# Performance work log

Measured on AMD Instinct MI355X. Metric: run time of the kernel, lower is better.

## Reference

```python
import jax, jax.numpy as jnp
import numpy as np

N_IN = 512
N_OUT = 256
T = 2048
B = 32


def setup_inputs() -> dict:
    key = jax.random.key(0)
    ks = jax.random.split(key, 9)
    s_in = 1.0 / np.sqrt(N_IN)
    inp = {
        "xt": jax.random.normal(ks[0], (T, B, N_IN), dtype=jnp.float32),
        "ct_forward": jax.random.normal(ks[1], (1, B, N_OUT), dtype=jnp.float32),
        # weights stored torch-style as [out, in]
        "Wx": jax.random.uniform(ks[2], (N_OUT, N_IN), jnp.float32, -s_in, s_in),
        "Wf": jax.random.uniform(ks[3], (N_OUT, N_IN), jnp.float32, -s_in, s_in),
        "bf": jax.random.uniform(ks[4], (N_OUT,), jnp.float32, -s_in, s_in),
        "Wr": jax.random.uniform(ks[5], (N_OUT, N_IN), jnp.float32, -s_in, s_in),
        "br": jax.random.uniform(ks[6], (N_OUT,), jnp.float32, -s_in, s_in),
        "Wc": jax.random.uniform(ks[7], (N_OUT, N_IN), jnp.float32, -s_in, s_in),
        "bc": jax.random.uniform(ks[8], (N_OUT,), jnp.float32, -s_in, s_in),
    }
    return inp


def reference(xt, ct_forward, Wx, Wf, bf, Wr, br, Wc, bc):
    # Batched projections over all timesteps (the GEMM part of SRU).
    x_proj = jnp.einsum("tbi,oi->tbo", xt, Wx)              # [T,B,n_out]
    f = jax.nn.sigmoid(jnp.einsum("tbi,oi->tbo", xt, Wf) + bf)
    r = jax.nn.sigmoid(jnp.einsum("tbi,oi->tbo", xt, Wr) + br)
    cx = jnp.einsum("tbi,oi->tbo", xt, Wc) + bc

    def step(c, inp):
        x_t, ft, rt, cxt = inp
        c = ft * c + (1.0 - ft) * x_t
        h = rt * jnp.tanh(c) + (1.0 - rt) * cxt
        return c, h

    c_final, ht = jax.lax.scan(step, ct_forward[0], (x_proj, f, r, cx))
    # dropout=0.0 -> identity; forward returns (ht, ct)
    return ht, c_final
```

## Files before the change

### kernel.cpp

```cpp
#include <hip/hip_runtime.h>
#include <stdint.h>

#define T_STEPS 2048
#define BATCH   32
#define NIN     512
#define NOUT    256
#define MROWS   (T_STEPS*BATCH)
#define BO      (BATCH*NOUT)
#define NCHUNK  32
#define CHLEN   (T_STEPS/NCHUNK)

typedef _Float16 f16x8 __attribute__((ext_vector_type(8)));
typedef _Float16 f16x4 __attribute__((ext_vector_type(4)));
typedef float    fx4   __attribute__((ext_vector_type(4)));

#define LDSP(p) ((__attribute__((address_space(3))) void*)(p))
#define GLBP(p) ((const __attribute__((address_space(1))) void*)(p))

#define BAR()       asm volatile("s_barrier" ::: "memory")
#define WAITLGKM0() do { asm volatile("s_waitcnt lgkmcnt(0)" ::: "memory"); __builtin_amdgcn_sched_barrier(0); } while(0)
#define WAITVM(n)   do { asm volatile("s_waitcnt vmcnt(" #n ")" ::: "memory"); __builtin_amdgcn_sched_barrier(0); } while(0)

__global__ __launch_bounds__(256) void convert_x(
    const float* __restrict__ xt, _Float16* __restrict__ xh)
{
    long i = ((long)blockIdx.x * 256 + threadIdx.x) * 8;
    float4 v0 = *(const float4*)(xt + i);
    float4 v1 = *(const float4*)(xt + i + 4);
    f16x8 h;
    h[0] = (_Float16)v0.x; h[1] = (_Float16)v0.y;
    h[2] = (_Float16)v0.z; h[3] = (_Float16)v0.w;
    h[4] = (_Float16)v1.x; h[5] = (_Float16)v1.y;
    h[6] = (_Float16)v1.z; h[7] = (_Float16)v1.w;
    *(f16x8*)(xh + i) = h;
}

__global__ __launch_bounds__(256) void convert_w(
    const float* __restrict__ Wx, const float* __restrict__ Wf,
    const float* __restrict__ Wr, const float* __restrict__ Wc,
    _Float16* __restrict__ Wcat)
{
    int idx = blockIdx.x * 256 + threadIdx.x;
    int n  = idx >> 7;
    int k4 = (idx & 127) * 4;
    int g = n >> 8, o = n & 255;
    const float* W = (g == 0) ? Wx : (g == 1) ? Wf : (g == 2) ? Wr : Wc;
    float4 v = *(const float4*)(W + o * NIN + k4);
    f16x4 h;
    h[0] = (_Float16)v.x; h[1] = (_Float16)v.y;
    h[2] = (_Float16)v.z; h[3] = (_Float16)v.w;
    *(f16x4*)(Wcat + n * NIN + k4) = h;
}

#define BM 256
#define BN 256
#define BK 64
#define NKT (NIN / BK)

__global__ __launch_bounds__(512) void gemm_proj(
    const _Float16* __restrict__ xh,
    const _Float16* __restrict__ Wcat,
    const float* __restrict__ bfv, const float* __restrict__ brv, const float* __restrict__ bcv,
    _Float16* __restrict__ xp_h, _Float16* __restrict__ f_h,
    _Float16* __restrict__ r_h,  _Float16* __restrict__ cx_h)
{
    __shared__ char lds[131072];

    const int tid  = threadIdx.x;
    const int lane = tid & 63;
    const int w    = tid >> 6;
    const int wrq  = w >> 2;
    const int wcq  = w & 3;
    const int lr = lane & 15, lk = lane >> 4;

    int wg = (blockIdx.x & 7) * 128 + (blockIdx.x >> 3);
    const int  rowblk = wg >> 2;
    const int  cg     = wg & 3;
    const long m0 = (long)rowblk * BM;
    const int  n0 = cg * BN;

    const int rl8  = lane >> 3;
    const int scol = (((lane & 7) ^ rl8) << 4);
    const char* baseA = (const char*)xh   + (m0 + w * 8 + rl8) * 1024 + scol;
    const char* baseB = (const char*)Wcat + ((long)(n0 + w * 8 + rl8)) * 1024 + scol;

#define STAGE_A(t, h) do {                                                   \
        char* _d = lds + ((t) & 1) * 32768 + (h) * 16384 + w * 1024;         \
        const char* _s = baseA + (long)(h) * 131072 + (t) * 128;             \
        __builtin_amdgcn_global_load_lds(GLBP(_s),         LDSP(_d),        16, 0, 0); \
        __builtin_amdgcn_global_load_lds(GLBP(_s + 65536), LDSP(_d + 8192), 16, 0, 0); \
    } while (0)
#define STAGE_B(t, h) do {                                                   \
        char* _d = lds + 65536 + ((t) & 1) * 32768 + (h) * 16384 + w * 1024; \
        const char* _s = baseB + (long)(h) * 131072 + (t) * 128;             \
        __builtin_amdgcn_global_load_lds(GLBP(_s),         LDSP(_d),        16, 0, 0); \
        __builtin_amdgcn_global_load_lds(GLBP(_s + 65536), LDSP(_d + 8192), 16, 0, 0); \
    } while (0)

    fx4 acc[2][2][4][2];
    #pragma unroll
    for (int a = 0; a < 2; ++a)
        #pragma unroll
        for (int b = 0; b < 2; ++b)
            #pragma unroll
            for (int c = 0; c < 4; ++c)
                #pragma unroll
                for (int d = 0; d < 2; ++d)
                    acc[a][b][c][d] = (fx4){0.f, 0.f, 0.f, 0.f};

    f16x8 Ar[4][2];
    f16x8 B0r[2][2];
    f16x8 B1r[2][2];

#define READ_A(c2, h) do {                                                   \
        _Pragma("unroll")                                                    \
        for (int mf = 0; mf < 4; ++mf) {                                     \
            int rl = wrq * 64 + mf * 16 + lr;                                \
            int rb = (c2) * 32768 + (h) * 16384 + rl * 128;                  \
            _Pragma("unroll")                                                \
            for (int kk = 0; kk < 2; ++kk)                                   \
                Ar[mf][kk] = *(const f16x8*)(lds + rb +                      \
                    ((kk * 64 + lk * 16) ^ ((rl & 7) << 4)));                \
        }                                                                    \
    } while (0)
#define READ_B(c2, h, dst) do {                                              \
        _Pragma("unroll")                                                    \
        for (int nf = 0; nf < 2; ++nf) {                                     \
            int rl = wcq * 32 + nf * 16 + lr;                                \
            int rb = 65536 + (c2) * 32768 + (h) * 16384 + rl * 128;          \
            _Pragma("unroll")                                                \
            for (int kk = 0; kk < 2; ++kk)                                   \
                dst[nf][kk] = *(const f16x8*)(lds + rb +                     \
                    ((kk * 64 + lk * 16) ^ ((rl & 7) << 4)));                \
        }                                                                    \
    } while (0)
#define MMACC(Qr, Qc, Br) do {                                               \
        __builtin_amdgcn_s_setprio(1);                                       \
        _Pragma("unroll")                                                    \
        for (int kk = 0; kk < 2; ++kk)                                       \
            _Pragma("unroll")                                                \
            for (int mf = 0; mf < 4; ++mf)                                   \
                _Pragma("unroll")                                            \
                for (int nf = 0; nf < 2; ++nf)                               \
                    acc[Qr][Qc][mf][nf] = __builtin_amdgcn_mfma_f32_16x16x32_f16( \
                        Ar[mf][kk], Br[nf][kk], acc[Qr][Qc][mf][nf], 0, 0, 0);    \
        __builtin_amdgcn_s_setprio(0);                                       \
    } while (0)

    STAGE_A(0, 0); STAGE_B(0, 0); STAGE_B(0, 1); STAGE_A(0, 1);
    STAGE_A(1, 0); STAGE_B(1, 0);
    WAITVM(4);
    BAR();

    for (int t = 0; t < NKT; ++t) {
        const int c2 = t & 1;
        READ_A(c2, 0);
        READ_B(c2, 0, B0r);
        if (t + 1 < NKT) STAGE_B(t + 1, 1);
        BAR();
        WAITLGKM0();
        MMACC(0, 0, B0r);
        BAR();
        READ_B(c2, 1, B1r);
        if (t + 1 < NKT) STAGE_A(t + 1, 1);
        BAR();
        WAITLGKM0();
        MMACC(0, 1, B1r);
        BAR();
        READ_A(c2, 1);
        if (t + 2 < NKT) STAGE_A(t + 2, 0);
        BAR();
        WAITLGKM0();
        MMACC(1, 0, B0r);
        BAR();
        if (t + 2 < NKT) STAGE_B(t + 2, 0);
        BAR();
        MMACC(1, 1, B1r);
        if (t < NKT - 2)       WAITVM(4);
        else if (t == NKT - 2) WAITVM(0);
        BAR();
    }

    const int g = cg;
    _Float16* outp = (g == 0) ? xp_h : (g == 1) ? f_h : (g == 2) ? r_h : cx_h;
    const float* bias = (g == 1) ? bfv : (g == 2) ? brv : (g == 3) ? bcv : nullptr;
    #pragma unroll
    for (int Qr = 0; Qr < 2; ++Qr) {
        #pragma unroll
        for (int Qc = 0; Qc < 2; ++Qc) {
            #pragma unroll
            for (int mf = 0; mf < 4; ++mf) {
                #pragma unroll
                for (int nf = 0; nf < 2; ++nf) {
                    int o = Qc * 128 + wcq * 32 + nf * 16 + lr;
                    float bv = (g == 0) ? 0.f : bias[o];
                    #pragma unroll
                    for (int j = 0; j < 4; ++j) {
                        long row = m0 + Qr * 128 + wrq * 64 + mf * 16 + lk * 4 + j;
                        float v = acc[Qr][Qc][mf][nf][j] + bv;
                        _Float16 hv;
                        if (g == 1 || g == 2) {
                            float e = __expf(-v);
                            hv = (_Float16)(__builtin_amdgcn_rcpf(1.0f + e));
                        } else {
                            hv = (_Float16)v;
                        }
                        outp[row * NOUT + o] = hv;
                    }
                }
            }
        }
    }
}

__global__ __launch_bounds__(256) void chunk_scan_a(
    const _Float16* __restrict__ f_h, const _Float16* __restrict__ xp_h,
    float* __restrict__ chunkA, float* __restrict__ chunkB)
{
    int tid = blockIdx.x * 256 + threadIdx.x;
    int chunk = tid >> 13;
    int bo = tid & (BO - 1);
    long base = (long)chunk * CHLEN * BO + bo;
    float a = 1.f, cc = 0.f;
    #pragma unroll 4
    for (int s = 0; s < CHLEN; ++s) {
        long i = base + (long)s * BO;
        float fv = (float)f_h[i];
        float xv = (float)xp_h[i];
        cc = fv * cc + (1.f - fv) * xv;
        a *= fv;
    }
    chunkA[tid] = a;
    chunkB[tid] = cc;
}

__global__ __launch_bounds__(256) void chunk_prop(
    const float* __restrict__ ct0,
    const float* __restrict__ chunkA, const float* __restrict__ chunkB,
    float* __restrict__ cin, float* __restrict__ c_final)
{
    int bo = blockIdx.x * 256 + threadIdx.x;
    float c = ct0[bo];
    #pragma unroll
    for (int ch = 0; ch < NCHUNK; ++ch) {
        cin[ch * BO + bo] = c;
        c = chunkA[ch * BO + bo] * c + chunkB[ch * BO + bo];
    }
    c_final[bo] = c;
}

__global__ __launch_bounds__(256) void chunk_scan_h(
    const _Float16* __restrict__ xp_h, const _Float16* __restrict__ f_h,
    const _Float16* __restrict__ r_h,  const _Float16* __restrict__ cx_h,
    const float* __restrict__ cin, float* __restrict__ ht)
{
    int tid = blockIdx.x * 256 + threadIdx.x;
    int chunk = tid >> 13;
    int bo = tid & (BO - 1);
    long base = (long)chunk * CHLEN * BO + bo;
    float c = cin[tid];
    #pragma unroll 4
    for (int s = 0; s < CHLEN; ++s) {
        long i = base + (long)s * BO;
        float fv = (float)f_h[i];
        float xv = (float)xp_h[i];
        float rv = (float)r_h[i];
        float cxv = (float)cx_h[i];
        c = fv * c + (1.f - fv) * xv;
        float e = __expf(2.f * c);
        float th = (e - 1.f) * __builtin_amdgcn_rcpf(e + 1.f);
        ht[i] = rv * th + (1.f - rv) * cxv;
    }
}

extern "C" void kernel_launch(void* const* d_in, const int* in_sizes, int n_in,
                              void* d_out, int out_size, void* d_ws, size_t ws_size,
                              hipStream_t stream) {
    const float* xt  = (const float*)d_in[0];
    const float* ct0 = (const float*)d_in[1];
    const float* Wx  = (const float*)d_in[2];
    const float* Wf  = (const float*)d_in[3];
    const float* bf_ = (const float*)d_in[4];
    const float* Wr  = (const float*)d_in[5];
    const float* br_ = (const float*)d_in[6];
    const float* Wc  = (const float*)d_in[7];
    const float* bc_ = (const float*)d_in[8];

    float* ht      = (float*)d_out;
    float* c_final = ht + (size_t)MROWS * NOUT;

    char* ws = (char*)d_ws;
    _Float16* Wcat = (_Float16*)ws;
    _Float16* xh   = (_Float16*)(ws + (1 << 20));
    _Float16* xp_h = xh + (size_t)MROWS * NIN;
    _Float16* f_h  = xp_h + (size_t)MROWS * NOUT;
    _Float16* r_h  = f_h  + (size_t)MROWS * NOUT;
    _Float16* cx_h = r_h  + (size_t)MROWS * NOUT;
    float* chunkA  = (float*)(cx_h + (size_t)MROWS * NOUT);
    float* chunkB  = chunkA + NCHUNK * BO;
    float* cin     = chunkB + NCHUNK * BO;

    convert_w<<<512, 256, 0, stream>>>(Wx, Wf, Wr, Wc, Wcat);
    convert_x<<<(MROWS * NIN / 8) / 256, 256, 0, stream>>>(xt, xh);
    gemm_proj<<<(MROWS / BM) * 4, 512, 0, stream>>>(
        xh, Wcat, bf_, br_, bc_, xp_h, f_h, r_h, cx_h);
    chunk_scan_a<<<(NCHUNK * BO) / 256, 256, 0, stream>>>(f_h, xp_h, chunkA, chunkB);
    chunk_prop<<<BO / 256, 256, 0, stream>>>(ct0, chunkA, chunkB, cin, c_final);
    chunk_scan_h<<<(NCHUNK * BO) / 256, 256, 0, stream>>>(xp_h, f_h, r_h, cx_h, cin, ht);
}
```

Baseline: 194.5 us.

## Make GEMM persistent over four row tiles and vectorize epilogue stores

The projection GEMM now launches 256 workgroups, each walking four consecutive 256-row tiles with one continuous software pipeline across tile boundaries, writing results and zeroing accumulators every eight k-steps. This removes per-tile pipeline warmup and drain and launch overhead. MFMA operands are swapped so each lane holds four consecutive output columns, letting the epilogue issue 8-byte f16x4 stores and float4 bias loads instead of scalar 2-byte stores. The cost is fewer workgroups (256 on a 256-CU device, one wave of work) and an epilogue placed inside the main loop, which adds register pressure.

```diff
diff --git a/kernel.cpp b/kernel.cpp
--- a/kernel.cpp
+++ b/kernel.cpp
@@ -55,7 +55,7 @@
 #define BM 256
 #define BN 256
 #define BK 64
-#define NKT (NIN / BK)
+#define NGT 32
 
 __global__ __launch_bounds__(512) void gemm_proj(
     const _Float16* __restrict__ xh,
@@ -73,10 +73,10 @@
     const int wcq  = w & 3;
     const int lr = lane & 15, lk = lane >> 4;
 
-    int wg = (blockIdx.x & 7) * 128 + (blockIdx.x >> 3);
-    const int  rowblk = wg >> 2;
-    const int  cg     = wg & 3;
-    const long m0 = (long)rowblk * BM;
+    int wg = (blockIdx.x & 7) * 32 + (blockIdx.x >> 3);
+    const int  cg   = wg & 3;
+    const int  mgrp = wg >> 2;
+    const long m0 = (long)mgrp * 1024;
     const int  n0 = cg * BN;
 
     const int rl8  = lane >> 3;
@@ -84,15 +84,16 @@
     const char* baseA = (const char*)xh   + (m0 + w * 8 + rl8) * 1024 + scol;
     const char* baseB = (const char*)Wcat + ((long)(n0 + w * 8 + rl8)) * 1024 + scol;
 
-#define STAGE_A(t, h) do {                                                   \
-        char* _d = lds + ((t) & 1) * 32768 + (h) * 16384 + w * 1024;         \
-        const char* _s = baseA + (long)(h) * 131072 + (t) * 128;             \
+#define STAGE_A(g, h) do {                                                   \
+        char* _d = lds + ((g) & 1) * 32768 + (h) * 16384 + w * 1024;         \
+        const char* _s = baseA + (long)((g) >> 3) * 262144                   \
+                         + ((g) & 7) * 128 + (long)(h) * 131072;             \
         __builtin_amdgcn_global_load_lds(GLBP(_s),         LDSP(_d),        16, 0, 0); \
         __builtin_amdgcn_global_load_lds(GLBP(_s + 65536), LDSP(_d + 8192), 16, 0, 0); \
     } while (0)
-#define STAGE_B(t, h) do {                                                   \
-        char* _d = lds + 65536 + ((t) & 1) * 32768 + (h) * 16384 + w * 1024; \
-        const char* _s = baseB + (long)(h) * 131072 + (t) * 128;             \
+#define STAGE_B(g, h) do {                                                   \
+        char* _d = lds + 65536 + ((g) & 1) * 32768 + (h) * 16384 + w * 1024; \
+        const char* _s = baseB + ((g) & 7) * 128 + (long)(h) * 131072;       \
         __builtin_amdgcn_global_load_lds(GLBP(_s),         LDSP(_d),        16, 0, 0); \
         __builtin_amdgcn_global_load_lds(GLBP(_s + 65536), LDSP(_d + 8192), 16, 0, 0); \
     } while (0)
@@ -143,69 +144,79 @@
                 _Pragma("unroll")                                            \
                 for (int nf = 0; nf < 2; ++nf)                               \
                     acc[Qr][Qc][mf][nf] = __builtin_amdgcn_mfma_f32_16x16x32_f16( \
-                        Ar[mf][kk], Br[nf][kk], acc[Qr][Qc][mf][nf], 0, 0, 0);    \
+                        Br[nf][kk], Ar[mf][kk], acc[Qr][Qc][mf][nf], 0, 0, 0);    \
         __builtin_amdgcn_s_setprio(0);                                       \
     } while (0)
+
+    const int g_out = cg;
+    _Float16* outp = (g_out == 0) ? xp_h : (g_out == 1) ? f_h : (g_out == 2) ? r_h : cx_h;
+    const float* bias = (g_out == 1) ? bfv : (g_out == 2) ? brv : (g_out == 3) ? bcv : nullptr;
 
     STAGE_A(0, 0); STAGE_B(0, 0); STAGE_B(0, 1); STAGE_A(0, 1);
     STAGE_A(1, 0); STAGE_B(1, 0);
     WAITVM(4);
     BAR();
 
-    for (int t = 0; t < NKT; ++t) {
-        const int c2 = t & 1;
+    for (int g = 0; g < NGT; ++g) {
+        const int c2 = g & 1;
         READ_A(c2, 0);
         READ_B(c2, 0, B0r);
-        if (t + 1 < NKT) STAGE_B(t + 1, 1);
+        if (g + 1 < NGT) STAGE_B(g + 1, 1);
         BAR();
         WAITLGKM0();
         MMACC(0, 0, B0r);
         BAR();
         READ_B(c2, 1, B1r);
-        if (t + 1 < NKT) STAGE_A(t + 1, 1);
+        if (g + 1 < NGT) STAGE_A(g + 1, 1);
         BAR();
         WAITLGKM0();
         MMACC(0, 1, B1r);
         BAR();
         READ_A(c2, 1);
-        if (t + 2 < NKT) STAGE_A(t + 2, 0);
+        if (g + 2 < NGT) STAGE_A(g + 2, 0);
         BAR();
         WAITLGKM0();
         MMACC(1, 0, B0r);
         BAR();
-        if (t + 2 < NKT) STAGE_B(t + 2, 0);
+        if (g + 2 < NGT) STAGE_B(g + 2, 0);
         BAR();
         MMACC(1, 1, B1r);
-        if (t < NKT - 2)       WAITVM(4);
-        else if (t == NKT - 2) WAITVM(0);
-        BAR();
-    }
-
-    const int g = cg;
-    _Float16* outp = (g == 0) ? xp_h : (g == 1) ? f_h : (g == 2) ? r_h : cx_h;
-    const float* bias = (g == 1) ? bfv : (g == 2) ? brv : (g == 3) ? bcv : nullptr;
-    #pragma unroll
-    for (int Qr = 0; Qr < 2; ++Qr) {
-        #pragma unroll
-        for (int Qc = 0; Qc < 2; ++Qc) {
+        if (g < NGT - 2)       WAITVM(4);
+        else if (g == NGT - 2) WAITVM(0);
+        BAR();
+
+        if ((g & 7) == 7) {
+            const long mbase = m0 + (long)(g >> 3) * 256;
             #pragma unroll
-            for (int mf = 0; mf < 4; ++mf) {
+            for (int Qr = 0; Qr < 2; ++Qr) {
                 #pragma unroll
-                for (int nf = 0; nf < 2; ++nf) {
-                    int o = Qc * 128 + wcq * 32 + nf * 16 + lr;
-                    float bv = (g == 0) ? 0.f : bias[o];
+                for (int Qc = 0; Qc < 2; ++Qc) {
                     #pragma unroll
-                    for (int j = 0; j < 4; ++j) {
-                        long row = m0 + Qr * 128 + wrq * 64 + mf * 16 + lk * 4 + j;
-                        float v = acc[Qr][Qc][mf][nf][j] + bv;
-                        _Float16 hv;
-                        if (g == 1 || g == 2) {
-                            float e = __expf(-v);
-                            hv = (_Float16)(__builtin_amdgcn_rcpf(1.0f + e));
-                        } else {
-                            hv = (_Float16)v;
+                    for (int nf = 0; nf < 2; ++nf) {
+                        const int ob = Qc * 128 + wcq * 32 + nf * 16 + lk * 4;
+                        float4 bv4 = (g_out == 0) ? (float4){0.f, 0.f, 0.f, 0.f}
+                                                  : *(const float4*)(bias + ob);
+                        #pragma unroll
+                        for (int mf = 0; mf < 4; ++mf) {
+                            long row = mbase + Qr * 128 + wrq * 64 + mf * 16 + lr;
+                            fx4 v = acc[Qr][Qc][mf][nf];
+                            f16x4 hv;
+                            if (g_out == 1 || g_out == 2) {
+                                float p0 = v[0] + bv4.x, p1 = v[1] + bv4.y;
+                                float p2 = v[2] + bv4.z, p3 = v[3] + bv4.w;
+                                hv[0] = (_Float16)(__builtin_amdgcn_rcpf(1.0f + __expf(-p0)));
+                                hv[1] = (_Float16)(__builtin_amdgcn_rcpf(1.0f + __expf(-p1)));
+                                hv[2] = (_Float16)(__builtin_amdgcn_rcpf(1.0f + __expf(-p2)));
+                                hv[3] = (_Float16)(__builtin_amdgcn_rcpf(1.0f + __expf(-p3)));
+                            } else {
+                                hv[0] = (_Float16)(v[0] + bv4.x);
+                                hv[1] = (_Float16)(v[1] + bv4.y);
+                                hv[2] = (_Float16)(v[2] + bv4.z);
+                                hv[3] = (_Float16)(v[3] + bv4.w);
+                            }
+                            *(f16x4*)(outp + row * NOUT + ob) = hv;
+                            acc[Qr][Qc][mf][nf] = (fx4){0.f, 0.f, 0.f, 0.f};
                         }
-                        outp[row * NOUT + o] = hv;
                     }
                 }
             }
@@ -302,7 +313,7 @@
 
     convert_w<<<512, 256, 0, stream>>>(Wx, Wf, Wr, Wc, Wcat);
     convert_x<<<(MROWS * NIN / 8) / 256, 256, 0, stream>>>(xt, xh);
-    gemm_proj<<<(MROWS / BM) * 4, 512, 0, stream>>>(
+    gemm_proj<<<256, 512, 0, stream>>>(
         xh, Wcat, bf_, br_, bc_, xp_h, f_h, r_h, cx_h);
     chunk_scan_a<<<(NCHUNK * BO) / 256, 256, 0, stream>>>(f_h, xp_h, chunkA, chunkB);
     chunk_prop<<<BO / 256, 256, 0, stream>>>(ct0, chunkA, chunkB, cin, c_final);
```

Result: no change. 192.9 us (-0.8%).
